# Kernel optimization log

Hardware: AMD Instinct MI355X
Metric: run time of the kernel (lower is better)

Reference implementation:

```python
import jax, jax.numpy as jnp
import numpy as np

EPS = 1e-12


def _l2norm(v):
    return v / (jnp.linalg.norm(v) + EPS)


def _sn(W, u):
    """One-step power-iteration spectral normalization (torch spectral_norm, 1x1 conv weight).
    W: (out, in), u: (out,). u/v are treated as buffers (no grad)."""
    Wm = W.reshape(W.shape[0], -1)
    v = _l2norm(Wm.T @ u)
    u2 = _l2norm(Wm @ v)
    u2 = jax.lax.stop_gradient(u2)
    v = jax.lax.stop_gradient(v)
    sigma = u2 @ (Wm @ v)
    return W / sigma


def _maxpool2(x):
    # 2x2 max pool, stride 2, NCHW
    N, C, H, W = x.shape
    return x.reshape(N, C, H // 2, 2, W // 2, 2).max(axis=(3, 5))


def setup_inputs() -> dict:
    key = jax.random.key(0)
    ks = jax.random.split(key, 10)
    N, C, H, W = 16, 256, 64, 64
    s = 0.05  # keep logits moderate
    return {
        "x": jax.random.normal(ks[0], (N, C, H, W), dtype=jnp.float32),
        "Wt": jax.random.normal(ks[1], (C >> 3, C), dtype=jnp.float32) * s,
        "Wp": jax.random.normal(ks[2], (C >> 3, C), dtype=jnp.float32) * s,
        "Wg": jax.random.normal(ks[3], (C >> 1, C), dtype=jnp.float32) * s,
        "Wo": jax.random.normal(ks[4], (C, C >> 1), dtype=jnp.float32) * s,
        "ut": jax.random.normal(ks[5], (C >> 3,), dtype=jnp.float32),
        "up": jax.random.normal(ks[6], (C >> 3,), dtype=jnp.float32),
        "ug": jax.random.normal(ks[7], (C >> 1,), dtype=jnp.float32),
        "uo": jax.random.normal(ks[8], (C,), dtype=jnp.float32),
        "gamma": jnp.float32(0.1),  # nonzero so attention branch is exercised
    }


def reference(x, Wt, Wp, Wg, Wo, ut, up, ug, uo, gamma):
    N, C, H, W = x.shape
    L = H * W          # location_num
    Ld = L // 4        # downsampled_num
    # 1x1 convs as channel einsums with spectrally-normalized weights
    theta = jnp.einsum('oc,nchw->nohw', _sn(Wt, ut), x).reshape(N, C >> 3, L)
    phi = _maxpool2(jnp.einsum('oc,nchw->nohw', _sn(Wp, up), x)).reshape(N, C >> 3, Ld)
    attn = jax.nn.softmax(jnp.einsum('ncl,ncm->nlm', theta, phi), axis=-1)  # (N, L, Ld)
    g = _maxpool2(jnp.einsum('oc,nchw->nohw', _sn(Wg, ug), x)).reshape(N, C >> 1, Ld)
    attn_g = jnp.einsum('ncm,nlm->ncl', g, attn).reshape(N, C >> 1, H, W)
    attn_g = jnp.einsum('oc,nchw->nohw', _sn(Wo, uo), attn_g)
    return x + gamma * attn_g
```

## Files before the change

kernel.cpp:

```cpp
#include <hip/hip_runtime.h>
#include <math.h>

#define EPS 1e-12f

typedef unsigned short ushort_t;
typedef __attribute__((ext_vector_type(8))) short short8;
typedef __attribute__((ext_vector_type(4))) float f32x4;
typedef __attribute__((ext_vector_type(4))) unsigned short ushort4v;
typedef __attribute__((ext_vector_type(2))) unsigned int uint2v;
typedef __attribute__((ext_vector_type(4))) unsigned int uint32x4;

#define WS_WB_F 0
#define WS_WO_F 24576
#define WS_TH_F 40960
#define WS_PH_F 1089536
#define WS_G_F  1351680

__device__ __forceinline__ ushort_t f2bf(float f) {
  unsigned int u = __float_as_uint(f);
  u += 0x7fffu + ((u >> 16) & 1u);
  return (ushort_t)(u >> 16);
}
__device__ __forceinline__ float bf2f(ushort_t u) {
  return __uint_as_float(((unsigned int)u) << 16);
}
__device__ __forceinline__ unsigned int pack_bfrh(float lo, float hi) {
  unsigned int a = __float_as_uint(lo) + 0x8000u;
  unsigned int b = __float_as_uint(hi) + 0x8000u;
  return (a >> 16) | (b & 0xffff0000u);
}
__device__ __forceinline__ float exp2_hw(float x) {
  float r;
  asm("v_exp_f32 %0, %1" : "=v"(r) : "v"(x));
  return r;
}

__device__ __forceinline__ void gload_lds16(const ushort_t* g, ushort_t* l) {
  __builtin_amdgcn_global_load_lds(
      (const __attribute__((address_space(1))) unsigned int*)g,
      (__attribute__((address_space(3))) unsigned int*)l, 16, 0, 0);
}

__device__ __forceinline__ float block_reduce_sum(float v, float* red) {
  int t = threadIdx.x;
  red[t] = v;
  __syncthreads();
  #pragma unroll
  for (int s = 128; s > 0; s >>= 1) {
    if (t < s) red[t] += red[t + s];
    __syncthreads();
  }
  float r = red[0];
  __syncthreads();
  return r;
}

__global__ __launch_bounds__(256) void sn_kernel(
    const float* __restrict__ Wt, const float* __restrict__ Wp,
    const float* __restrict__ Wg, const float* __restrict__ Wo,
    const float* __restrict__ ut, const float* __restrict__ up,
    const float* __restrict__ ug, const float* __restrict__ uo,
    float* __restrict__ ws) {
  __shared__ float red[256];
  __shared__ float ub[256];
  __shared__ float vb[256];
  const float* W; const float* u; int O, Ci;
  switch (blockIdx.x) {
    case 0:  W = Wt; u = ut; O = 32;  Ci = 256; break;
    case 1:  W = Wp; u = up; O = 32;  Ci = 256; break;
    case 2:  W = Wg; u = ug; O = 128; Ci = 256; break;
    default: W = Wo; u = uo; O = 256; Ci = 128; break;
  }
  int t = threadIdx.x;
  if (t < O) ub[t] = u[t];
  __syncthreads();
  float tv = 0.f;
  if (t < Ci) {
    for (int o = 0; o < O; o++) tv += W[o * Ci + t] * ub[o];
  }
  float nt2 = block_reduce_sum((t < Ci) ? tv * tv : 0.f, red);
  float ntn = sqrtf(nt2);
  if (t < Ci) vb[t] = tv / (ntn + EPS);
  __syncthreads();
  float sv = 0.f;
  if (t < O) {
    const float* Wr = W + (size_t)t * Ci;
    for (int c = 0; c < Ci; c += 4) {
      float4 wv = *(const float4*)(Wr + c);
      sv += wv.x * vb[c] + wv.y * vb[c + 1] + wv.z * vb[c + 2] + wv.w * vb[c + 3];
    }
  }
  float ss = block_reduce_sum((t < O) ? sv * sv : 0.f, red);
  float ns = sqrtf(ss);
  float sigma = ss / (ns + EPS);
  float inv = 1.f / sigma;
  if (blockIdx.x == 0) inv *= 1.44269504088896f;
  int total = O * Ci;
  if (blockIdx.x == 3) {
    ushort_t* dst = (ushort_t*)(ws + WS_WO_F);
    for (int i = t; i < total; i += 256) {
      int o = i >> 7, c = i & 127;
      int oct = o >> 4, l16o = o & 15, kc = c >> 5, cl = c & 31;
      int kap = (cl < 16) ? ((cl >> 2) * 8 + (cl & 3))
                          : (((cl >> 2) & 3) * 8 + 4 + (cl & 3));
      dst[(((kc * 16 + oct) * 64 + (kap >> 3) * 16 + l16o) << 3) + (kap & 7)] =
          f2bf(W[i] * inv);
    }
  } else {
    int base_row = (blockIdx.x == 0) ? 0 : (blockIdx.x == 1 ? 32 : 64);
    ushort_t* dst = (ushort_t*)(ws + WS_WB_F);
    for (int i = t; i < total; i += 256) {
      int o = i >> 8, c = i & 255;
      int og = base_row + o;
      int mtg = og >> 4, l16o = og & 15, kc = c >> 5, qd = (c >> 3) & 3, j = c & 7;
      dst[(((mtg * 8 + kc) * 64 + qd * 16 + l16o) << 3) + j] = f2bf(W[i] * inv);
    }
  }
}

__global__ __launch_bounds__(256, 2) void proj_mfma(
    const float* __restrict__ x, const ushort_t* __restrict__ wb,
    ushort_t* __restrict__ theta_b, ushort_t* __restrict__ phi_b,
    ushort_t* __restrict__ g_fb) {
  __shared__ ushort_t xb[128 * 264];
  const int t = threadIdx.x;
  const int n = blockIdx.y;
  const int l0 = blockIdx.x * 128;
  const float* xn = x + ((size_t)n * 256) * 4096 + l0;
  {
    const int lrel = t & 127;
    const int half = t >> 7;
    #pragma unroll 4
    for (int ch = 0; ch < 16; ++ch) {
      int chunk = half * 16 + ch;
      short8 v;
      #pragma unroll
      for (int j = 0; j < 8; ++j) {
        float f = xn[(size_t)(chunk * 8 + j) * 4096 + lrel];
        v[j] = (short)f2bf(f);
      }
      *(short8*)(&xb[lrel * 264 + chunk * 8]) = v;
    }
  }
  __syncthreads();
  const int w = t >> 6;
  const int lane = t & 63;
  const int quad = lane >> 4;
  const int l16 = lane & 15;
  const int rowA = (w * 16 + l16) * 264;
  const int rowB = (64 + w * 16 + l16) * 264;
  const int hd = blockIdx.x;
  #pragma unroll 1
  for (int pass = 0; pass < 2; ++pass) {
    f32x4 accA[6], accB[6];
    #pragma unroll
    for (int i = 0; i < 6; ++i) {
      accA[i] = (f32x4){0.f, 0.f, 0.f, 0.f};
      accB[i] = (f32x4){0.f, 0.f, 0.f, 0.f};
    }
    #pragma unroll
    for (int kc = 0; kc < 8; ++kc) {
      short8 bA = *(const short8*)(&xb[rowA + kc * 32 + quad * 8]);
      short8 bB = *(const short8*)(&xb[rowB + kc * 32 + quad * 8]);
      #pragma unroll
      for (int mt = 0; mt < 6; ++mt) {
        int mtg = pass * 6 + mt;
        short8 aW = *(const short8*)(wb + (((size_t)(mtg * 8 + kc) * 64 + lane) << 3));
        accA[mt] = __builtin_amdgcn_mfma_f32_16x16x32_bf16(aW, bA, accA[mt], 0, 0, 0);
        accB[mt] = __builtin_amdgcn_mfma_f32_16x16x32_bf16(aW, bB, accB[mt], 0, 0, 0);
      }
    }
    #pragma unroll
    for (int mt = 0; mt < 6; ++mt) {
      int mtg = pass * 6 + mt;
      if (mtg < 2) {
        int lA = l0 + w * 16 + l16;
        ushort4v vA, vB;
        #pragma unroll
        for (int r = 0; r < 4; ++r) { vA[r] = f2bf(accA[mt][r]); vB[r] = f2bf(accB[mt][r]); }
        *(ushort4v*)(theta_b + ((size_t)n * 4096 + lA) * 32 + mtg * 16 + quad * 4) = vA;
        *(ushort4v*)(theta_b + ((size_t)n * 4096 + lA + 64) * 32 + mtg * 16 + quad * 4) = vB;
      } else {
        float pm[4];
        #pragma unroll
        for (int r = 0; r < 4; ++r) {
          float v = fmaxf(accA[mt][r], accB[mt][r]);
          v = fmaxf(v, __shfl_xor(v, 1));
          pm[r] = v;
        }
        if ((l16 & 1) == 0) {
          int rr = l16 >> 1;
          if (mtg < 4) {
            int mp = hd * 32 + ((rr & 4) ? 16 : 0) + w * 4 + (rr & 3);
            ushort4v vv;
            #pragma unroll
            for (int r = 0; r < 4; ++r) vv[r] = f2bf(pm[r]);
            *(ushort4v*)(phi_b + ((size_t)n * 1024 + mp) * 32 + (mtg - 2) * 16 + quad * 4) = vv;
          } else {
            size_t fb = (size_t)n * 131072 +
                        (size_t)((hd * 8 + (mtg - 4)) * 64 + w * 16 + quad * 4) * 8 + rr;
            #pragma unroll
            for (int r = 0; r < 4; ++r)
              g_fb[fb + (size_t)r * 8] = f2bf(pm[r]);
          }
        }
      }
    }
  }
}

__global__ __launch_bounds__(256, 4) void attn_mfma(
    const float* __restrict__ x,
    const ushort_t* __restrict__ theta_b,
    const ushort_t* __restrict__ phi_b,
    const ushort_t* __restrict__ g_fb,
    const ushort_t* __restrict__ Wo_fb,
    const float* __restrict__ gamma_p,
    float* __restrict__ out) {
  __shared__ __align__(16) unsigned char smem[34816];
  ushort_t* gbuf = (ushort_t*)smem;
  ushort_t* outb = (ushort_t*)smem;

  const int t = threadIdx.x;
  const int w = t >> 6;
  const int lane = t & 63;
  const int quad = lane >> 4;
  const int l16 = lane & 15;

  const int flat = blockIdx.y * 64 + blockIdx.x;
  const int nf = ((flat & 7) << 7) | (flat >> 3);
  const int n = nf >> 6;
  const int l0 = (nf & 63) << 6;
  const int lq = l0 + w * 16;

  const short8 bth = *(const short8*)(theta_b + ((size_t)n * 4096 + lq + l16) * 32 + quad * 8);
  const ushort_t* phiN = phi_b + (size_t)n * 1024 * 32;
  const ushort_t* gN   = g_fb + (size_t)n * 131072;

  f32x4 oacc[8];
  #pragma unroll
  for (int j = 0; j < 8; ++j) oacc[j] = (f32x4){0.f, 0.f, 0.f, 0.f};
  float M = -3.0e38f, L = 0.f;
  unsigned int pk[16];

  auto STAGE = [&](int mc) {
    const ushort_t* src = gN + (size_t)mc * 16384 + w * 8 * 512 + lane * 8;
    ushort_t* dst = gbuf + w * 8 * 512;
    #pragma unroll
    for (int b = 0; b < 8; ++b)
      gload_lds16(src + b * 512, dst + b * 512);
  };

  auto QKSM = [&](int mc) {
    const int m0 = mc * 128;
    const f32x4 z = (f32x4){0.f, 0.f, 0.f, 0.f};
    f32x4 st[8];
    #pragma unroll
    for (int i = 0; i < 8; ++i) {
      short8 aph = *(const short8*)(phiN + (size_t)(m0 + i * 16 + l16) * 32 + quad * 8);
      st[i] = __builtin_amdgcn_mfma_f32_16x16x32_bf16(aph, bth, z, 0, 0, 0);
    }
    f32x4 a0 = st[0], a1 = st[1], a2 = st[2], a3 = st[3];
    #pragma unroll
    for (int r = 0; r < 4; ++r) {
      a0[r] = fmaxf(a0[r], st[4][r]); a1[r] = fmaxf(a1[r], st[5][r]);
      a2[r] = fmaxf(a2[r], st[6][r]); a3[r] = fmaxf(a3[r], st[7][r]);
    }
    #pragma unroll
    for (int r = 0; r < 4; ++r) { a0[r] = fmaxf(a0[r], a2[r]); a1[r] = fmaxf(a1[r], a3[r]); }
    float mx = fmaxf(fmaxf(fmaxf(a0[0], a1[0]), fmaxf(a0[1], a1[1])),
                     fmaxf(fmaxf(a0[2], a1[2]), fmaxf(a0[3], a1[3])));
    mx = fmaxf(mx, __shfl_xor(mx, 16));
    mx = fmaxf(mx, __shfl_xor(mx, 32));
    float nm = fmaxf(M, mx);
    float alpha = exp2_hw(M - nm);
    M = nm;
    #pragma unroll
    for (int i = 0; i < 8; ++i) {
      #pragma unroll
      for (int r = 0; r < 4; ++r) st[i][r] = exp2_hw(st[i][r] - nm);
    }
    f32x4 s0 = st[0], s1 = st[1];
    #pragma unroll
    for (int r = 0; r < 4; ++r) {
      s0[r] += st[2][r] + st[4][r] + st[6][r];
      s1[r] += st[3][r] + st[5][r] + st[7][r];
    }
    float ps = (s0[0] + s1[0]) + (s0[1] + s1[1]) + (s0[2] + s1[2]) + (s0[3] + s1[3]);
    L = L * alpha + ps;
    #pragma unroll
    for (int j = 0; j < 8; ++j) {
      #pragma unroll
      for (int r = 0; r < 4; ++r) oacc[j][r] *= alpha;
    }
    #pragma unroll
    for (int i = 0; i < 8; ++i) {
      pk[2 * i]     = pack_bfrh(st[i][0], st[i][1]);
      pk[2 * i + 1] = pack_bfrh(st[i][2], st[i][3]);
    }
  };

  auto PV = [&]() {
    __builtin_amdgcn_s_setprio(1);
    #pragma unroll
    for (int s = 0; s < 4; ++s) {
      uint32x4 u = {pk[4 * s], pk[4 * s + 1], pk[4 * s + 2], pk[4 * s + 3]};
      short8 pb = __builtin_bit_cast(short8, u);
      #pragma unroll
      for (int j = 0; j < 8; ++j) {
        short8 gf = *(const short8*)(gbuf + (size_t)(s * 8 + j) * 512 + lane * 8);
        oacc[j] = __builtin_amdgcn_mfma_f32_16x16x32_bf16(gf, pb, oacc[j], 0, 0, 0);
      }
    }
    __builtin_amdgcn_s_setprio(0);
  };

  STAGE(0);
  QKSM(0);
  __syncthreads();
  #pragma unroll 1
  for (int mc = 0; mc < 8; ++mc) {
    PV();
    if (mc < 7) {
      __syncthreads();
      STAGE(mc + 1);
      QKSM(mc + 1);
      __syncthreads();
    }
  }
  __syncthreads();

  L += __shfl_xor(L, 16);
  L += __shfl_xor(L, 32);
  const float invL = 1.f / L;
  #pragma unroll
  for (int half = 0; half < 2; ++half) {
    f32x4 acc2[8];
    #pragma unroll
    for (int i = 0; i < 8; ++i) acc2[i] = (f32x4){0.f, 0.f, 0.f, 0.f};
    #pragma unroll
    for (int kc = 0; kc < 4; ++kc) {
      uint32x4 u;
      u[0] = pack_bfrh(oacc[2 * kc][0] * invL, oacc[2 * kc][1] * invL);
      u[1] = pack_bfrh(oacc[2 * kc][2] * invL, oacc[2 * kc][3] * invL);
      u[2] = pack_bfrh(oacc[2 * kc + 1][0] * invL, oacc[2 * kc + 1][1] * invL);
      u[3] = pack_bfrh(oacc[2 * kc + 1][2] * invL, oacc[2 * kc + 1][3] * invL);
      short8 aO = __builtin_bit_cast(short8, u);
      #pragma unroll
      for (int o8 = 0; o8 < 8; ++o8) {
        int oct = half * 8 + o8;
        short8 bw = *(const short8*)(Wo_fb + (((size_t)(kc * 16 + oct) * 64 + lane) << 3));
        acc2[o8] = __builtin_amdgcn_mfma_f32_16x16x32_bf16(aO, bw, acc2[o8], 0, 0, 0);
      }
    }
    #pragma unroll
    for (int o8 = 0; o8 < 8; ++o8) {
      int oct = half * 8 + o8;
      uint2v p2;
      p2[0] = pack_bfrh(acc2[o8][0], acc2[o8][1]);
      p2[1] = pack_bfrh(acc2[o8][2], acc2[o8][3]);
      *(uint2v*)(&outb[(oct * 16 + l16) * 68 + w * 16 + quad * 4]) = p2;
    }
  }
  __syncthreads();
  {
    const float gm = gamma_p[0];
    const int oc = (t >> 4);
    const int lch = (t & 15) * 4;
    #pragma unroll
    for (int ocg = 0; ocg < 16; ++ocg) {
      int row = ocg * 16 + oc;
      ushort4v ov = *(const ushort4v*)(&outb[row * 68 + lch]);
      const float* xp = x + ((size_t)n * 256 + row) * 4096 + l0 + lch;
      float* op = out + ((size_t)n * 256 + row) * 4096 + l0 + lch;
      float4 xv = *(const float4*)xp;
      float4 v;
      v.x = xv.x + gm * bf2f(ov[0]);
      v.y = xv.y + gm * bf2f(ov[1]);
      v.z = xv.z + gm * bf2f(ov[2]);
      v.w = xv.w + gm * bf2f(ov[3]);
      *(float4*)op = v;
    }
  }
}

extern "C" void kernel_launch(void* const* d_in, const int* in_sizes, int n_in,
                              void* d_out, int out_size, void* d_ws, size_t ws_size,
                              hipStream_t stream) {
  const float* x  = (const float*)d_in[0];
  const float* Wt = (const float*)d_in[1];
  const float* Wp = (const float*)d_in[2];
  const float* Wg = (const float*)d_in[3];
  const float* Wo = (const float*)d_in[4];
  const float* ut = (const float*)d_in[5];
  const float* up = (const float*)d_in[6];
  const float* ug = (const float*)d_in[7];
  const float* uo = (const float*)d_in[8];
  const float* gamma = (const float*)d_in[9];
  float* ws  = (float*)d_ws;
  float* out = (float*)d_out;

  ushort_t* wb      = (ushort_t*)(ws + WS_WB_F);
  ushort_t* Wo_b    = (ushort_t*)(ws + WS_WO_F);
  ushort_t* theta_b = (ushort_t*)(ws + WS_TH_F);
  ushort_t* phi_b   = (ushort_t*)(ws + WS_PH_F);
  ushort_t* g_fb    = (ushort_t*)(ws + WS_G_F);

  sn_kernel<<<4, 256, 0, stream>>>(Wt, Wp, Wg, Wo, ut, up, ug, uo, ws);
  proj_mfma<<<dim3(32, 16), 256, 0, stream>>>(x, wb, theta_b, phi_b, g_fb);
  attn_mfma<<<dim3(64, 16), 256, 0, stream>>>(x, theta_b, phi_b, g_fb, Wo_b, gamma, out);
}
```

Baseline: 204.9 us.

## Load x fragments directly into registers and add lazy softmax rescaling

The projection kernel no longer stages x through a large shared-memory tile. Each lane loads its bf16 MFMA fragments straight from global memory into registers, the work is split into four passes of three M-tiles, and launch bounds rise to 4 blocks per CU to raise occupancy. The attention kernel's online softmax now skips the max reduction and accumulator rescale unless some lane's max exceeds the running max by more than 8 (log2 units). This trades extra uncoalesced global loads and the risk of larger exp values for less LDS traffic and fewer shuffles and multiplies.

```diff
diff --git a/kernel.cpp b/kernel.cpp
--- a/kernel.cpp
+++ b/kernel.cpp
@@ -118,61 +118,63 @@
   }
 }
 
-__global__ __launch_bounds__(256, 2) void proj_mfma(
+__global__ __launch_bounds__(256, 4) void proj_mfma(
     const float* __restrict__ x, const ushort_t* __restrict__ wb,
     ushort_t* __restrict__ theta_b, ushort_t* __restrict__ phi_b,
     ushort_t* __restrict__ g_fb) {
-  __shared__ ushort_t xb[128 * 264];
   const int t = threadIdx.x;
   const int n = blockIdx.y;
-  const int l0 = blockIdx.x * 128;
-  const float* xn = x + ((size_t)n * 256) * 4096 + l0;
-  {
-    const int lrel = t & 127;
-    const int half = t >> 7;
-    #pragma unroll 4
-    for (int ch = 0; ch < 16; ++ch) {
-      int chunk = half * 16 + ch;
-      short8 v;
-      #pragma unroll
-      for (int j = 0; j < 8; ++j) {
-        float f = xn[(size_t)(chunk * 8 + j) * 4096 + lrel];
-        v[j] = (short)f2bf(f);
-      }
-      *(short8*)(&xb[lrel * 264 + chunk * 8]) = v;
-    }
-  }
-  __syncthreads();
+  const int hd = blockIdx.x;
+  const int l0 = hd * 128;
   const int w = t >> 6;
   const int lane = t & 63;
   const int quad = lane >> 4;
   const int l16 = lane & 15;
-  const int rowA = (w * 16 + l16) * 264;
-  const int rowB = (64 + w * 16 + l16) * 264;
-  const int hd = blockIdx.x;
+  const float* xn = x + (size_t)n * 256 * 4096;
+  const int pxA = l0 + w * 16 + l16;
+  const int pxB = pxA + 64;
+
+  short8 fA[8], fB[8];
   #pragma unroll 1
-  for (int pass = 0; pass < 2; ++pass) {
-    f32x4 accA[6], accB[6];
-    #pragma unroll
-    for (int i = 0; i < 6; ++i) {
+  for (int kc = 0; kc < 8; ++kc) {
+    float a[8], b[8];
+    #pragma unroll
+    for (int j = 0; j < 8; ++j) {
+      const float* cp = xn + (size_t)(kc * 32 + quad * 8 + j) * 4096;
+      a[j] = cp[pxA];
+      b[j] = cp[pxB];
+    }
+    uint32x4 ua, ub;
+    #pragma unroll
+    for (int p = 0; p < 4; ++p) {
+      ua[p] = pack_bfrh(a[2 * p], a[2 * p + 1]);
+      ub[p] = pack_bfrh(b[2 * p], b[2 * p + 1]);
+    }
+    fA[kc] = __builtin_bit_cast(short8, ua);
+    fB[kc] = __builtin_bit_cast(short8, ub);
+  }
+
+  #pragma unroll 1
+  for (int sp = 0; sp < 4; ++sp) {
+    f32x4 accA[3], accB[3];
+    #pragma unroll
+    for (int i = 0; i < 3; ++i) {
       accA[i] = (f32x4){0.f, 0.f, 0.f, 0.f};
       accB[i] = (f32x4){0.f, 0.f, 0.f, 0.f};
     }
     #pragma unroll
     for (int kc = 0; kc < 8; ++kc) {
-      short8 bA = *(const short8*)(&xb[rowA + kc * 32 + quad * 8]);
-      short8 bB = *(const short8*)(&xb[rowB + kc * 32 + quad * 8]);
       #pragma unroll
-      for (int mt = 0; mt < 6; ++mt) {
-        int mtg = pass * 6 + mt;
+      for (int mt = 0; mt < 3; ++mt) {
+        int mtg = sp * 3 + mt;
         short8 aW = *(const short8*)(wb + (((size_t)(mtg * 8 + kc) * 64 + lane) << 3));
-        accA[mt] = __builtin_amdgcn_mfma_f32_16x16x32_bf16(aW, bA, accA[mt], 0, 0, 0);
-        accB[mt] = __builtin_amdgcn_mfma_f32_16x16x32_bf16(aW, bB, accB[mt], 0, 0, 0);
+        accA[mt] = __builtin_amdgcn_mfma_f32_16x16x32_bf16(aW, fA[kc], accA[mt], 0, 0, 0);
+        accB[mt] = __builtin_amdgcn_mfma_f32_16x16x32_bf16(aW, fB[kc], accB[mt], 0, 0, 0);
       }
     }
     #pragma unroll
-    for (int mt = 0; mt < 6; ++mt) {
-      int mtg = pass * 6 + mt;
+    for (int mt = 0; mt < 3; ++mt) {
+      int mtg = sp * 3 + mt;
       if (mtg < 2) {
         int lA = l0 + w * 16 + l16;
         ushort4v vA, vB;
@@ -268,17 +270,25 @@
     }
     #pragma unroll
     for (int r = 0; r < 4; ++r) { a0[r] = fmaxf(a0[r], a2[r]); a1[r] = fmaxf(a1[r], a3[r]); }
-    float mx = fmaxf(fmaxf(fmaxf(a0[0], a1[0]), fmaxf(a0[1], a1[1])),
-                     fmaxf(fmaxf(a0[2], a1[2]), fmaxf(a0[3], a1[3])));
-    mx = fmaxf(mx, __shfl_xor(mx, 16));
-    mx = fmaxf(mx, __shfl_xor(mx, 32));
-    float nm = fmaxf(M, mx);
-    float alpha = exp2_hw(M - nm);
-    M = nm;
+    float mlane = fmaxf(fmaxf(fmaxf(a0[0], a1[0]), fmaxf(a0[1], a1[1])),
+                        fmaxf(fmaxf(a0[2], a1[2]), fmaxf(a0[3], a1[3])));
+    if (!__all(mlane <= M + 8.0f)) {
+      float mx = fmaxf(mlane, __shfl_xor(mlane, 16));
+      mx = fmaxf(mx, __shfl_xor(mx, 32));
+      float nm = fmaxf(M, mx);
+      float al = exp2_hw(M - nm);
+      M = nm;
+      L *= al;
+      #pragma unroll
+      for (int j = 0; j < 8; ++j) {
+        #pragma unroll
+        for (int r = 0; r < 4; ++r) oacc[j][r] *= al;
+      }
+    }
     #pragma unroll
     for (int i = 0; i < 8; ++i) {
       #pragma unroll
-      for (int r = 0; r < 4; ++r) st[i][r] = exp2_hw(st[i][r] - nm);
+      for (int r = 0; r < 4; ++r) st[i][r] = exp2_hw(st[i][r] - M);
     }
     f32x4 s0 = st[0], s1 = st[1];
     #pragma unroll
@@ -286,13 +296,7 @@
       s0[r] += st[2][r] + st[4][r] + st[6][r];
       s1[r] += st[3][r] + st[5][r] + st[7][r];
     }
-    float ps = (s0[0] + s1[0]) + (s0[1] + s1[1]) + (s0[2] + s1[2]) + (s0[3] + s1[3]);
-    L = L * alpha + ps;
-    #pragma unroll
-    for (int j = 0; j < 8; ++j) {
-      #pragma unroll
-      for (int r = 0; r < 4; ++r) oacc[j][r] *= alpha;
-    }
+    L += (s0[0] + s1[0]) + (s0[1] + s1[1]) + (s0[2] + s1[2]) + (s0[3] + s1[3]);
     #pragma unroll
     for (int i = 0; i < 8; ++i) {
       pk[2 * i]     = pack_bfrh(st[i][0], st[i][1]);
```

Result: slower. 258.1 us (+26.0%).
